# Performance work log

Hardware: AMD Instinct MI355X
Metric: run time of the kernel (lower is better)

## Reference

```python
import jax, jax.numpy as jnp
import numpy as np

B, N, C, NC = 16, 49, 512, 12  # batch, spatial tokens, channels, num AU classes
EPS = 1e-5


def bn(h, axes):
    # torch BatchNorm (training mode, gamma=1, beta=0): biased batch stats
    m = h.mean(axes, keepdims=True)
    v = h.var(axes, keepdims=True)
    return (h - m) * jax.lax.rsqrt(v + EPS)


def cross_attn(y, x, qw, qb, kw, kb, vw, vb):
    # CrossAttn: q from y, k/v from x; attention over the token (N) axis
    q = y @ qw.T + qb            # (..., N, C//2)
    k = x @ kw.T + kb
    v = x @ vw.T + vb            # (..., N, C)
    scale = (C // 2) ** -0.5
    attn = jax.nn.softmax(jnp.einsum('...ij,...kj->...ik', q, k) * scale, axis=-1)
    return attn @ v


def _gnn_block(x, edge, A, Bm, E, U, V):
    # One ME-GraphAU GCN message-passing block.
    # x: (B, NC, C) node feats; edge: (B, NC*NC, C), edge (i,j) stored at i*NC+j
    b = x.shape[0]
    Vix = x @ A.T   # gathered at end node j of each edge
    Vjx = x @ Bm.T  # gathered at start node i of each edge
    msg = (Vjx[:, :, None, :] + Vix[:, None, :, :]).reshape(b, NC * NC, C) + edge @ E.T
    edge = edge + jax.nn.relu(bn(msg, (0, 2)))              # bne: per-edge-slot stats
    e = jax.nn.sigmoid(edge).reshape(b, NC, NC, C)
    e = jax.nn.softmax(e, axis=2)                            # softmax over target j
    Ujx = x @ V.T                                            # start-node features
    agg = (e * Ujx[:, :, None, :]).sum(axis=1) / NC          # sum over source i -> node j
    xn = x @ U.T + agg
    x = jax.nn.relu(x + bn(xn, (0, 2)))                      # bnv: per-class stats
    return x, edge


def _forward(x, cls_w, cls_b, attn_qw, attn_qb, attn_kw, attn_kb, attn_vw, attn_vb,
             ep_w, ep_b, gnn_w, mlp_w1, mlp_b1, mlp_w2, mlp_b2, mlp_w3, mlp_b3,
             final_w, final_b):
    b = x.shape[0]
    # per-class LinearBlocks, batched: (B, NC, N, C)
    h = jnp.einsum('bnc,koc->bkno', x, cls_w) + cls_b[None, :, None, :]
    f_u = jax.nn.relu(bn(h, (0, 2)))           # each class has its own BN over (B, N)
    f_v = f_u.mean(-2)                          # (B, NC, C)

    # GEM edge extractor
    g = jnp.broadcast_to(x[:, None], (b, NC, N, C))
    feat = cross_attn(f_u, g, attn_qw[0], attn_qb[0], attn_kw[0], attn_kb[0], attn_vw[0], attn_vb[0])
    # feat_end[i*NC+j] = feat[i]; feat_start[i*NC+j] = feat[j]
    feat_end = jnp.broadcast_to(feat[:, :, None], (b, NC, NC, N, C)).reshape(b, NC * NC, N, C)
    feat_start = jnp.broadcast_to(feat[:, None, :], (b, NC, NC, N, C)).reshape(b, NC * NC, N, C)
    feat2 = cross_attn(feat_start, feat_end, attn_qw[1], attn_qb[1], attn_kw[1], attn_kb[1], attn_vw[1], attn_vb[1])
    edge = bn(feat2 @ ep_w.T + ep_b, (0, 2, 3))  # BatchNorm2d(NC*NC): stats over (B, N, C)
    f_e = edge.mean(-2)                           # (B, NC*NC, C)

    # two GCN message-passing blocks
    U1, V1, A1, B1, E1, U2, V2, A2, B2, E2 = gnn_w
    f_v, f_e = _gnn_block(f_v, f_e, A1, B1, E1, U1, V1)
    f_v, f_e = _gnn_block(f_v, f_e, A2, B2, E2, U2, V2)

    # vectorized pairwise class-link head (feed_type='vertex+edge'), pairs i<j in loop order
    iu, ju = np.triu_indices(NC, 1)
    edges = jnp.concatenate([f_e[:, iu * NC + ju], f_e[:, ju * NC + iu]], axis=-1)  # (B, 66, 2C)
    nodes = jnp.concatenate([f_v[:, iu], f_v[:, ju]], axis=-1)                       # (B, 66, 2C)

    def mlp(z, i):
        z = jax.nn.relu(z @ mlp_w1[i].T + mlp_b1[i])
        z = jax.nn.relu(z @ mlp_w2[i].T + mlp_b2[i])
        return z @ mlp_w3[i].T + mlp_b3[i]

    ed = mlp(edges, 0)
    nd = mlp(nodes, 1)
    return jnp.concatenate([ed, nd], axis=-1) @ final_w.T + final_b  # (B, 66, 4)


def setup_inputs() -> dict:
    key = jax.random.key(0)
    ks = jax.random.split(key, 12)

    def w(k, shape, fan_in):
        return jax.random.normal(k, shape, jnp.float32) * (2.0 / fan_in) ** 0.5

    return dict(
        x=jax.random.normal(ks[0], (B, N, C), jnp.float32),
        cls_w=w(ks[1], (NC, C, C), C),          # per-class Linear (out, in)
        cls_b=jnp.zeros((NC, C), jnp.float32),
        attn_qw=w(ks[2], (2, C // 2, C), C),    # [0]=FAM, [1]=ARM
        attn_qb=jnp.zeros((2, C // 2), jnp.float32),
        attn_kw=w(ks[3], (2, C // 2, C), C),
        attn_kb=jnp.zeros((2, C // 2), jnp.float32),
        attn_vw=w(ks[4], (2, C, C), C),
        attn_vb=jnp.zeros((2, C), jnp.float32),
        ep_w=w(ks[5], (C, C), C),               # GEM edge_proj
        ep_b=jnp.zeros((C,), jnp.float32),
        gnn_w=w(ks[6], (10, C, C), C),          # U1,V1,A1,B1,E1,U2,V2,A2,B2,E2 (no bias)
        mlp_w1=w(ks[7], (2, C, 2 * C), 2 * C),  # [0]=edge_fc_*, [1]=node_fc_*
        mlp_b1=jnp.zeros((2, C), jnp.float32),
        mlp_w2=w(ks[8], (2, C // 2, C), C),
        mlp_b2=jnp.zeros((2, C // 2), jnp.float32),
        mlp_w3=w(ks[9], (2, 4, C // 2), C // 2),
        mlp_b3=jnp.zeros((2, 4), jnp.float32),
        final_w=w(ks[10], (4, 8), 8),
        final_b=jnp.zeros((4,), jnp.float32),
    )


def reference(x, cls_w, cls_b, attn_qw, attn_qb, attn_kw, attn_kb, attn_vw, attn_vb,
              ep_w, ep_b, gnn_w, mlp_w1, mlp_b1, mlp_w2, mlp_b2, mlp_w3, mlp_b3,
              final_w, final_b):
    return _forward(x, cls_w, cls_b, attn_qw, attn_qb, attn_kw, attn_kb, attn_vw, attn_vb,
                    ep_w, ep_b, gnn_w, mlp_w1, mlp_b1, mlp_w2, mlp_b2, mlp_w3, mlp_b3,
                    final_w, final_b)
```

## Files before the change

kernel.cpp:

```cpp
#include <hip/hip_runtime.h>

#define BN_EPS 1e-5f

typedef float f32x4 __attribute__((ext_vector_type(4)));
typedef short s16x8 __attribute__((ext_vector_type(8)));

__device__ __forceinline__ short f2bf(float f) {
    unsigned u = __builtin_bit_cast(unsigned, f);
    u = (u + 0x7fffu + ((u >> 16) & 1u)) >> 16;
    return (short)u;
}

__global__ __launch_bounds__(256) void cvt_multi_kernel(
    const float* __restrict__ s0, const float* __restrict__ s1, const float* __restrict__ s2,
    const float* __restrict__ s3, const float* __restrict__ s4, const float* __restrict__ s5,
    const float* __restrict__ s6, const float* __restrict__ s7, const float* __restrict__ s8,
    short* __restrict__ d0, short* __restrict__ d1, short* __restrict__ d2,
    short* __restrict__ d3, short* __restrict__ d4, short* __restrict__ d5,
    short* __restrict__ d6, short* __restrict__ d7, short* __restrict__ d8)
{
    int idx = blockIdx.x * 256 + threadIdx.x;
    const float* src; short* dst; int local;
    if      (idx <   50176) { src = s0; dst = d0; local = idx; }
    else if (idx <  443392) { src = s1; dst = d1; local = idx -   50176; }
    else if (idx <  476160) { src = s2; dst = d2; local = idx -  443392; }
    else if (idx <  508928) { src = s3; dst = d3; local = idx -  476160; }
    else if (idx <  574464) { src = s4; dst = d4; local = idx -  508928; }
    else if (idx <  607232) { src = s5; dst = d5; local = idx -  574464; }
    else if (idx <  934912) { src = s6; dst = d6; local = idx -  607232; }
    else if (idx < 1065984) { src = s7; dst = d7; local = idx -  934912; }
    else if (idx < 1098752) { src = s8; dst = d8; local = idx - 1065984; }
    else return;
    const float4* s4p = reinterpret_cast<const float4*>(src) + (size_t)local * 2;
    float4 a = s4p[0], b = s4p[1];
    s16x8 v;
    v[0] = f2bf(a.x); v[1] = f2bf(a.y); v[2] = f2bf(a.z); v[3] = f2bf(a.w);
    v[4] = f2bf(b.x); v[5] = f2bf(b.y); v[6] = f2bf(b.z); v[7] = f2bf(b.w);
    reinterpret_cast<s16x8*>(dst)[local] = v;
}

template<int OMODE>
__global__ __launch_bounds__(256) void mfma_linear_kernel(
    const short* __restrict__ X, int Xstride,
    const short* __restrict__ W, int Wstride,
    const float* __restrict__ bias, int bstride,
    void* __restrict__ Yv, int Ystride,
    int R, int Cin, int Cout, int relu)
{
    const int mat = blockIdx.z;
    X += (size_t)mat * Xstride;
    W += (size_t)mat * Wstride;
    const float* bp = bias ? bias + mat * bstride : nullptr;
    float* Yf = (float*)Yv + (size_t)mat * Ystride;
    short* Ys = (short*)Yv + (size_t)mat * Ystride;

    const int r0 = blockIdx.y * 64;
    const int o0 = blockIdx.x * 64;

    __shared__ short As[64 * 40];
    __shared__ short Bs[64 * 40];

    const int tid = threadIdx.x;
    const int lane = tid & 63;
    const int wave = tid >> 6;
    const int wr = wave >> 1, wc = wave & 1;
    const int l15 = lane & 15;
    const int lk = lane >> 4;

    const int trow = tid >> 2;
    const int tseg = (tid & 3) * 8;

    f32x4 acc[2][2] = {};

    const int arow = r0 + trow;
    const bool aok = arow < R;
    const short* xrow = X + (size_t)arow * Cin + tseg;
    const short* wrow = W + (size_t)(o0 + trow) * Cin + tseg;

    for (int k0 = 0; k0 < Cin; k0 += 32) {
        s16x8 av = {};
        if (aok) av = *reinterpret_cast<const s16x8*>(xrow + k0);
        s16x8 bv = *reinterpret_cast<const s16x8*>(wrow + k0);
        *reinterpret_cast<s16x8*>(&As[trow * 40 + tseg]) = av;
        *reinterpret_cast<s16x8*>(&Bs[trow * 40 + tseg]) = bv;
        __syncthreads();

        s16x8 af[2], bf[2];
        #pragma unroll
        for (int mi = 0; mi < 2; mi++)
            af[mi] = *reinterpret_cast<const s16x8*>(&As[(wr * 32 + mi * 16 + l15) * 40 + lk * 8]);
        #pragma unroll
        for (int ni = 0; ni < 2; ni++)
            bf[ni] = *reinterpret_cast<const s16x8*>(&Bs[(wc * 32 + ni * 16 + l15) * 40 + lk * 8]);
        #pragma unroll
        for (int mi = 0; mi < 2; mi++)
            #pragma unroll
            for (int ni = 0; ni < 2; ni++)
                acc[mi][ni] = __builtin_amdgcn_mfma_f32_16x16x32_bf16(af[mi], bf[ni], acc[mi][ni], 0, 0, 0);
        __syncthreads();
    }

    #pragma unroll
    for (int mi = 0; mi < 2; mi++) {
        #pragma unroll
        for (int ni = 0; ni < 2; ni++) {
            int col = o0 + wc * 32 + ni * 16 + l15;
            int row0 = r0 + wr * 32 + mi * 16 + lk * 4;
            float bb = bp ? bp[col] : 0.f;
            #pragma unroll
            for (int r = 0; r < 4; r++) {
                int row = row0 + r;
                if (row < R) {
                    float v = acc[mi][ni][r] + bb;
                    if (relu) v = fmaxf(v, 0.f);
                    if (OMODE == 0) {
                        Yf[(size_t)row * Cout + col] = v;
                    } else if (OMODE == 1) {
                        Ys[(size_t)row * Cout + col] = f2bf(v);
                    } else {
                        int t = row / 49, n = row - t * 49;
                        Ys[((size_t)t * 512 + col) * 64 + n] = f2bf(v);
                    }
                }
            }
        }
    }
}

__global__ __launch_bounds__(256) void bn1_partial_kernel(
    const float* __restrict__ h, float* __restrict__ bsum, float* __restrict__ bsq)
{
    int k = blockIdx.x;
    int part = blockIdx.y;
    int tid = threadIdx.x;
    #pragma unroll
    for (int half = 0; half < 2; half++) {
        int o = tid + half * 256;
        const float* base = h + (size_t)k * 401408 + (size_t)part * 98 * 512 + o;
        float s = 0.f, sq = 0.f;
        #pragma unroll 7
        for (int bn = 0; bn < 98; bn++) {
            float v = base[bn * 512];
            s += v; sq += v * v;
        }
        atomicAdd(&bsum[k * 512 + o], s);
        atomicAdd(&bsq[k * 512 + o], sq);
    }
}

__global__ __launch_bounds__(256) void fu_fv_kernel(
    const float* __restrict__ h, const float* __restrict__ bsum,
    const float* __restrict__ bsq, short* __restrict__ fu_bf,
    float* __restrict__ f_v, short* __restrict__ fv_bf)
{
    int b = blockIdx.x;
    int k = blockIdx.y;
    int tid = threadIdx.x;
    #pragma unroll
    for (int half = 0; half < 2; half++) {
        int o = tid + half * 256;
        float mu = bsum[k * 512 + o] * (1.f / 784.f);
        float var = bsq[k * 512 + o] * (1.f / 784.f) - mu * mu;
        float rs = rsqrtf(var + BN_EPS);
        const float* base = h + (size_t)(k * 16 + b) * 49 * 512 + o;
        short* obase = fu_bf + (size_t)(k * 16 + b) * 49 * 512 + o;
        float acc = 0.f;
        #pragma unroll 7
        for (int n = 0; n < 49; n++) {
            float v = (base[n * 512] - mu) * rs;
            v = fmaxf(v, 0.f);
            obase[n * 512] = f2bf(v);
            acc += v;
        }
        float fvv = acc * (1.f / 49.f);
        f_v[(b * 12 + k) * 512 + o] = fvv;
        fv_bf[(b * 12 + k) * 512 + o] = f2bf(fvv);
    }
}

__global__ __launch_bounds__(256) void attn1_kernel(
    const float* __restrict__ q1,
    const float* __restrict__ k1,
    const float* __restrict__ v1,
    short* __restrict__ feat)
{
    int b = blockIdx.x;
    int k = blockIdx.y;
    __shared__ float ks[49 * 260];
    __shared__ float Pt[49 * 56];
    int tid = threadIdx.x;
    const float* kb = k1 + b * 49 * 256;
    for (int e = tid; e < 49 * 256; e += 256) ks[(e >> 8) * 260 + (e & 255)] = kb[e];
    __syncthreads();
    const float* qb = q1 + (k * 16 + b) * 49 * 256;
    for (int e = tid; e < 49 * 49; e += 256) {
        int qi = e / 49, kj = e - qi * 49;
        const float4* q4 = reinterpret_cast<const float4*>(qb + qi * 256);
        const float4* k4 = reinterpret_cast<const float4*>(ks + kj * 260);
        float s = 0.f;
        #pragma unroll 8
        for (int d = 0; d < 64; d++) {
            float4 a = q4[d], c = k4[d];
            s += a.x * c.x + a.y * c.y + a.z * c.z + a.w * c.w;
        }
        Pt[kj * 56 + qi] = s * 0.0625f;
    }
    __syncthreads();
    if (tid < 196) {
        int qi = tid >> 2, sub = tid & 3;
        float ev[13];
        float m = -1e30f;
        #pragma unroll 13
        for (int t = 0; t < 13; t++) {
            int j = sub + t * 4;
            ev[t] = (j < 49) ? Pt[j * 56 + qi] : -1e30f;
            m = fmaxf(m, ev[t]);
        }
        m = fmaxf(m, __shfl_xor(m, 1));
        m = fmaxf(m, __shfl_xor(m, 2));
        float s = 0.f;
        #pragma unroll 13
        for (int t = 0; t < 13; t++) { ev[t] = __expf(ev[t] - m); s += ev[t]; }
        s += __shfl_xor(s, 1);
        s += __shfl_xor(s, 2);
        float inv = 1.f / s;
        #pragma unroll 13
        for (int t = 0; t < 13; t++) {
            int j = sub + t * 4;
            if (j < 49) Pt[j * 56 + qi] = ev[t] * inv;
        }
    }
    __syncthreads();
    const float* vb = v1 + b * 49 * 512;
    short* fb = feat + (size_t)(k * 16 + b) * 49 * 512;
    for (int qc = 0; qc < 49; qc += 8) {
        int nq = 49 - qc; if (nq > 8) nq = 8;
        float a0[8] = {}, a1[8] = {};
        for (int kj = 0; kj < 49; kj++) {
            float v0 = vb[kj * 512 + tid];
            float v1v = vb[kj * 512 + 256 + tid];
            const float4* pr = reinterpret_cast<const float4*>(&Pt[kj * 56 + qc]);
            float4 p0 = pr[0], p1 = pr[1];
            a0[0] += p0.x * v0; a1[0] += p0.x * v1v;
            a0[1] += p0.y * v0; a1[1] += p0.y * v1v;
            a0[2] += p0.z * v0; a1[2] += p0.z * v1v;
            a0[3] += p0.w * v0; a1[3] += p0.w * v1v;
            a0[4] += p1.x * v0; a1[4] += p1.x * v1v;
            a0[5] += p1.y * v0; a1[5] += p1.y * v1v;
            a0[6] += p1.z * v0; a1[6] += p1.z * v1v;
            a0[7] += p1.w * v0; a1[7] += p1.w * v1v;
        }
        #pragma unroll 8
        for (int u = 0; u < 8; u++) {
            if (u < nq) {
                fb[(qc + u) * 512 + tid] = f2bf(a0[u]);
                fb[(qc + u) * 512 + 256 + tid] = f2bf(a1[u]);
            }
        }
    }
}

__global__ __launch_bounds__(256) void attn2_mfma_kernel(
    const short* __restrict__ q2,
    const short* __restrict__ k2,
    const short* __restrict__ w2vT,
    const float* __restrict__ ep_b,
    float* __restrict__ fe_raw,
    float* __restrict__ stats)
{
    const int b = blockIdx.x, i = blockIdx.y;
    __shared__ short Vs[512 * 64];
    __shared__ float S[64 * 68];
    __shared__ short P[64 * 88];
    const int tid = threadIdx.x;
    const int lane = tid & 63, w = tid >> 6;
    const int l15 = lane & 15, lk = lane >> 4;

    {
        const float4* src = reinterpret_cast<const float4*>(w2vT + (size_t)((i * 16 + b) * 512) * 64);
        float4* dst = reinterpret_cast<float4*>(Vs);
        #pragma unroll
        for (int it = 0; it < 16; it++) {
            int c = tid + it * 256;
            int ch = c >> 3, c8 = c & 7;
            dst[(ch << 3) | (c8 ^ (ch & 7))] = src[c];
        }
        for (int idx = tid; idx < 64 * 88; idx += 256) P[idx] = 0;
    }
    const short* kb = k2 + (size_t)((i * 16 + b) * 49) * 256;
    __syncthreads();

    for (int j = 0; j < 12; j++) {
        const short* qb = q2 + (size_t)((j * 16 + b) * 49) * 256;
        {
            int qrow = w * 16 + l15; if (qrow > 48) qrow = 48;
            f32x4 sacc[4] = {};
            #pragma unroll
            for (int ks = 0; ks < 8; ks++) {
                s16x8 aq = *reinterpret_cast<const s16x8*>(qb + (size_t)qrow * 256 + ks * 32 + lk * 8);
                #pragma unroll
                for (int ni = 0; ni < 4; ni++) {
                    int krow = ni * 16 + l15; if (krow > 48) krow = 48;
                    s16x8 bk = *reinterpret_cast<const s16x8*>(kb + (size_t)krow * 256 + ks * 32 + lk * 8);
                    sacc[ni] = __builtin_amdgcn_mfma_f32_16x16x32_bf16(aq, bk, sacc[ni], 0, 0, 0);
                }
            }
            #pragma unroll
            for (int ni = 0; ni < 4; ni++)
                #pragma unroll
                for (int r = 0; r < 4; r++)
                    S[(w * 16 + lk * 4 + r) * 68 + ni * 16 + l15] = sacc[ni][r] * 0.0625f;
        }
        __syncthreads();

        if (tid < 196) {
            int qi = tid >> 2, sub = tid & 3;
            float ev[13];
            float m = -1e30f;
            #pragma unroll 13
            for (int t = 0; t < 13; t++) {
                int kk = sub + t * 4;
                ev[t] = (kk < 49) ? S[qi * 68 + kk] : -1e30f;
                m = fmaxf(m, ev[t]);
            }
            m = fmaxf(m, __shfl_xor(m, 1));
            m = fmaxf(m, __shfl_xor(m, 2));
            float s = 0.f;
            #pragma unroll 13
            for (int t = 0; t < 13; t++) { ev[t] = __expf(ev[t] - m); s += ev[t]; }
            s += __shfl_xor(s, 1);
            s += __shfl_xor(s, 2);
            float inv = 1.f / s;
            #pragma unroll 13
            for (int t = 0; t < 13; t++) {
                int kk = sub + t * 4;
                if (kk < 49) P[qi * 88 + kk] = f2bf(ev[t] * inv);
            }
        }
        __syncthreads();

        const int slot = i * 12 + j;
        float tot = 0.f, csq = 0.f;
        #pragma unroll
        for (int half = 0; half < 2; half++) {
            const int cb = half * 256 + w * 64;
            f32x4 pac[4][4] = {};
            #pragma unroll
            for (int ks = 0; ks < 2; ks++) {
                s16x8 bv[4];
                #pragma unroll
                for (int ni = 0; ni < 4; ni++) {
                    int ch = cb + ni * 16 + l15;
                    int boff = ((ch * 64 + ks * 32 + lk * 8) * 2) ^ ((ch & 7) << 4);
                    bv[ni] = *reinterpret_cast<const s16x8*>(reinterpret_cast<const char*>(Vs) + boff);
                }
                #pragma unroll
                for (int mi = 0; mi < 4; mi++) {
                    s16x8 ap = *reinterpret_cast<const s16x8*>(&P[(mi * 16 + l15) * 88 + ks * 32 + lk * 8]);
                    #pragma unroll
                    for (int ni = 0; ni < 4; ni++)
                        pac[mi][ni] = __builtin_amdgcn_mfma_f32_16x16x32_bf16(ap, bv[ni], pac[mi][ni], 0, 0, 0);
                }
            }
            #pragma unroll
            for (int ni = 0; ni < 4; ni++) {
                int col = cb + ni * 16 + l15;
                float bias = ep_b[col];
                float cs = 0.f;
                #pragma unroll
                for (int mi = 0; mi < 4; mi++) {
                    #pragma unroll
                    for (int r = 0; r < 4; r++) {
                        int row = mi * 16 + lk * 4 + r;
                        if (row < 49) {
                            float sv = pac[mi][ni][r] + bias;
                            cs += sv; csq += sv * sv;
                        }
                    }
                }
                tot += cs;
                cs += __shfl_xor(cs, 16);
                cs += __shfl_xor(cs, 32);
                if (lk == 0)
                    fe_raw[((size_t)b * 144 + slot) * 512 + col] = cs * (1.f / 49.f);
            }
        }
        tot += __shfl_xor(tot, 1);  tot += __shfl_xor(tot, 2);  tot += __shfl_xor(tot, 4);
        tot += __shfl_xor(tot, 8);  tot += __shfl_xor(tot, 16); tot += __shfl_xor(tot, 32);
        csq += __shfl_xor(csq, 1);  csq += __shfl_xor(csq, 2);  csq += __shfl_xor(csq, 4);
        csq += __shfl_xor(csq, 8);  csq += __shfl_xor(csq, 16); csq += __shfl_xor(csq, 32);
        if (lane == 0) {
            atomicAdd(&stats[slot * 2], tot);
            atomicAdd(&stats[slot * 2 + 1], csq);
        }
    }
}

__global__ __launch_bounds__(256) void edge_fin_kernel(
    const float* __restrict__ stats, float* __restrict__ fe, short* __restrict__ fe_bf)
{
    int s = blockIdx.x;
    const float inv = 1.f / 401408.f;
    float mu = stats[s * 2] * inv;
    float var = stats[s * 2 + 1] * inv - mu * mu;
    float rs = rsqrtf(var + BN_EPS);
    int tid = threadIdx.x;
    for (int b = 0; b < 16; b++) {
        float* p = fe + (b * 144 + s) * 512;
        short* pb = fe_bf + (b * 144 + s) * 512;
        #pragma unroll
        for (int half = 0; half < 2; half++) {
            int c = tid + half * 256;
            float nv = (p[c] - mu) * rs;
            p[c] = nv;
            pb[c] = f2bf(nv);
        }
    }
}

__global__ __launch_bounds__(256) void gnn_edge_kernel(
    const float* __restrict__ nodeproj,
    const float* __restrict__ eE,
    float* __restrict__ fe, short* __restrict__ fe_bf)
{
    int s = blockIdx.x;
    int i = s / 12, j = s - i * 12;
    int tid = threadIdx.x;
    const float* Vix = nodeproj + 2 * 98304;
    const float* Vjx = nodeproj + 3 * 98304;
    __shared__ float red[256];
    float msg[32];
    float sum = 0.f, sq = 0.f;
    int idx = 0;
    for (int b = 0; b < 16; b++) {
        #pragma unroll
        for (int half = 0; half < 2; half++) {
            int c = tid + half * 256;
            float v = Vjx[(b * 12 + i) * 512 + c] + Vix[(b * 12 + j) * 512 + c]
                    + eE[(b * 144 + s) * 512 + c];
            msg[idx++] = v;
            sum += v; sq += v * v;
        }
    }
    red[tid] = sum; __syncthreads();
    for (int t = 128; t > 0; t >>= 1) { if (tid < t) red[tid] += red[tid + t]; __syncthreads(); }
    float tsum = red[0]; __syncthreads();
    red[tid] = sq; __syncthreads();
    for (int t = 128; t > 0; t >>= 1) { if (tid < t) red[tid] += red[tid + t]; __syncthreads(); }
    float tsq = red[0];
    float mu = tsum * (1.f / 8192.f);
    float var = tsq * (1.f / 8192.f) - mu * mu;
    float rs = rsqrtf(var + BN_EPS);
    idx = 0;
    for (int b = 0; b < 16; b++) {
        #pragma unroll
        for (int half = 0; half < 2; half++) {
            int c = tid + half * 256;
            int o = (b * 144 + s) * 512 + c;
            float v = fmaxf((msg[idx++] - mu) * rs, 0.f);
            float nv = fe[o] + v;
            fe[o] = nv;
            fe_bf[o] = f2bf(nv);
        }
    }
}

__global__ __launch_bounds__(256) void gnn_agg_kernel(
    const float* __restrict__ fe,
    const float* __restrict__ nodeproj,
    float* __restrict__ xn_agg)
{
    int b = blockIdx.x;
    int i = blockIdx.y;
    int tid = threadIdx.x;
    const float* Ujx = nodeproj + 98304;
    #pragma unroll
    for (int half = 0; half < 2; half++) {
        int c = tid + half * 256;
        float sg[12];
        float m = -1e30f;
        #pragma unroll
        for (int j = 0; j < 12; j++) {
            float e = fe[(b * 144 + i * 12 + j) * 512 + c];
            float sv = 1.f / (1.f + __expf(-e));
            sg[j] = sv;
            m = fmaxf(m, sv);
        }
        float ssum = 0.f;
        #pragma unroll
        for (int j = 0; j < 12; j++) { float evv = __expf(sg[j] - m); sg[j] = evv; ssum += evv; }
        float wgt = Ujx[(b * 12 + i) * 512 + c] / ssum;
        #pragma unroll
        for (int j = 0; j < 12; j++)
            atomicAdd(&xn_agg[(b * 12 + j) * 512 + c], sg[j] * wgt);
    }
}

__global__ __launch_bounds__(256) void gnn_node_kernel(
    const float* __restrict__ xn_agg, const float* __restrict__ nodeproj,
    float* __restrict__ fv, short* __restrict__ fv_bf)
{
    int k = blockIdx.x;
    int tid = threadIdx.x;
    const float* Ux = nodeproj;
    __shared__ float red[256];
    float vals[32];
    float sum = 0.f, sq = 0.f;
    int idx = 0;
    for (int b = 0; b < 16; b++) {
        #pragma unroll
        for (int half = 0; half < 2; half++) {
            int c = tid + half * 256;
            int o = (b * 12 + k) * 512 + c;
            float v = Ux[o] + xn_agg[o] * (1.f / 12.f);
            vals[idx++] = v;
            sum += v; sq += v * v;
        }
    }
    red[tid] = sum; __syncthreads();
    for (int t = 128; t > 0; t >>= 1) { if (tid < t) red[tid] += red[tid + t]; __syncthreads(); }
    float tsum = red[0]; __syncthreads();
    red[tid] = sq; __syncthreads();
    for (int t = 128; t > 0; t >>= 1) { if (tid < t) red[tid] += red[tid + t]; __syncthreads(); }
    float tsq = red[0];
    float mu = tsum * (1.f / 8192.f);
    float var = tsq * (1.f / 8192.f) - mu * mu;
    float rs = rsqrtf(var + BN_EPS);
    idx = 0;
    for (int b = 0; b < 16; b++) {
        #pragma unroll
        for (int half = 0; half < 2; half++) {
            int c = tid + half * 256;
            int o = (b * 12 + k) * 512 + c;
            float v = (vals[idx++] - mu) * rs;
            float nv = fmaxf(fv[o] + v, 0.f);
            fv[o] = nv;
            fv_bf[o] = f2bf(nv);
        }
    }
}

__global__ __launch_bounds__(256) void pair_gather_kernel(
    const float* __restrict__ fe, const float* __restrict__ fv, short* __restrict__ pairX)
{
    int p = blockIdx.x;
    int b = blockIdx.y;
    int tid = threadIdx.x;
    int i = 0, rem = p;
    while (rem >= 11 - i) { rem -= 11 - i; i++; }
    int j = i + 1 + rem;
    short* e_out = pairX + (size_t)(b * 66 + p) * 1024;
    short* n_out = pairX + (size_t)1056 * 1024 + (size_t)(b * 66 + p) * 1024;
    const float* fe_ij = fe + (b * 144 + i * 12 + j) * 512;
    const float* fe_ji = fe + (b * 144 + j * 12 + i) * 512;
    const float* fv_i = fv + (b * 12 + i) * 512;
    const float* fv_j = fv + (b * 12 + j) * 512;
    #pragma unroll
    for (int half = 0; half < 2; half++) {
        int c = tid + half * 256;
        e_out[c] = f2bf(fe_ij[c]);
        e_out[512 + c] = f2bf(fe_ji[c]);
        n_out[c] = f2bf(fv_i[c]);
        n_out[512 + c] = f2bf(fv_j[c]);
    }
}

__global__ __launch_bounds__(256) void mlp3_kernel(
    const float* __restrict__ X,
    const float* __restrict__ w3,
    const float* __restrict__ b3,
    float* __restrict__ Y)
{
    int idx = blockIdx.x * 256 + threadIdx.x;
    if (idx >= 8448) return;
    int o = idx & 3;
    int r = (idx >> 2) % 1056;
    int m = idx / (4 * 1056);
    const float* x = X + (m * 1056 + r) * 256;
    const float* w = w3 + (m * 4 + o) * 256;
    float s = b3[m * 4 + o];
    #pragma unroll 8
    for (int c = 0; c < 256; c++) s += x[c] * w[c];
    Y[idx] = s;
}

__global__ __launch_bounds__(256) void final_kernel(
    const float* __restrict__ mid3,
    const float* __restrict__ fw,
    const float* __restrict__ fb,
    float* __restrict__ out)
{
    int idx = blockIdx.x * 256 + threadIdx.x;
    if (idx >= 4224) return;
    int o = idx & 3;
    int r = idx >> 2;
    const float* ed = mid3 + r * 4;
    const float* nd = mid3 + 1056 * 4 + r * 4;
    float s = fb[o];
    #pragma unroll
    for (int q = 0; q < 4; q++) s += ed[q] * fw[o * 8 + q];
    #pragma unroll
    for (int q = 0; q < 4; q++) s += nd[q] * fw[o * 8 + 4 + q];
    out[idx] = s;
}

extern "C" void kernel_launch(void* const* d_in, const int* in_sizes, int n_in,
                              void* d_out, int out_size, void* d_ws, size_t ws_size,
                              hipStream_t stream)
{
    const float* x      = (const float*)d_in[0];
    const float* cls_w  = (const float*)d_in[1];
    const float* cls_b  = (const float*)d_in[2];
    const float* qw     = (const float*)d_in[3];
    const float* qb     = (const float*)d_in[4];
    const float* kw     = (const float*)d_in[5];
    const float* kb     = (const float*)d_in[6];
    const float* vw     = (const float*)d_in[7];
    const float* vb     = (const float*)d_in[8];
    const float* ep_w   = (const float*)d_in[9];
    const float* ep_b   = (const float*)d_in[10];
    const float* gnn_w  = (const float*)d_in[11];
    const float* mlp_w1 = (const float*)d_in[12];
    const float* mlp_b1 = (const float*)d_in[13];
    const float* mlp_w2 = (const float*)d_in[14];
    const float* mlp_b2 = (const float*)d_in[15];
    const float* mlp_w3 = (const float*)d_in[16];
    const float* mlp_b3 = (const float*)d_in[17];
    const float* fin_w  = (const float*)d_in[18];
    const float* fin_b  = (const float*)d_in[19];
    float* out = (float*)d_out;
    float* ws = (float*)d_ws;

    float* A      = ws;
    float* q1b    = A + 4816896;
    float* k1b    = q1b + 2408448;
    float* v1b    = k1b + 200704;
    float* Bb     = v1b + 401408;
    float* Cb     = Bb + 3145728;
    float* fv     = Cb + 2408448;
    float* fvbf_f = fv + 98304;
    float* bn1m   = fvbf_f + 49152;
    float* bn1r   = bn1m + 6144;
    float* fe     = bn1r + 6144;
    float* febf_f = fe + 1179648;
    float* stats  = febf_f + 589824;
    float* xbf_f  = stats + 288;
    float* cwbf_f = xbf_f + 200704;
    float* qwbf_f = cwbf_f + 1572864;
    float* kwbf_f = qwbf_f + 131072;
    float* vwbf_f = kwbf_f + 131072;
    float* ewbf_f = vwbf_f + 262144;
    float* gwbf_f = ewbf_f + 131072;
    float* m1bf_f = gwbf_f + 1310720;
    float* m2bf_f = m1bf_f + 524288;

    short* xbf   = (short*)xbf_f;
    short* cwbf  = (short*)cwbf_f;
    short* qwbf  = (short*)qwbf_f;
    short* kwbf  = (short*)kwbf_f;
    short* vwbf  = (short*)vwbf_f;
    short* ewbf  = (short*)ewbf_f;
    short* gwbf  = (short*)gwbf_f;
    short* m1wbf = (short*)m1bf_f;
    short* m2wbf = (short*)m2bf_f;

    short* fubf   = (short*)Cb;
    short* featbf = (short*)Bb;
    short* q2bf   = (short*)A;
    short* k2bf   = (short*)A + 2408448;
    short* v2bf   = (short*)Cb;
    short* w2vT   = (short*)Bb;
    short* fvbf   = (short*)fvbf_f;
    short* febf   = (short*)febf_f;

    float* nodeproj = Cb;
    float* eE       = Cb + 393216;
    float* xn       = Cb + 1572864;
    short* pairXbf  = (short*)Cb;
    short* mid1bf   = (short*)Cb + 2162688;
    float* mid2     = Cb + 1622016;
    float* mid3     = Cb + 2162688;

    cvt_multi_kernel<<<4293, 256, 0, stream>>>(
        x, cls_w, qw, kw, vw, ep_w, gnn_w, mlp_w1, mlp_w2,
        xbf, cwbf, qwbf, kwbf, vwbf, ewbf, gwbf, m1wbf, m2wbf);

    mfma_linear_kernel<0><<<dim3(8, 13, 12), 256, 0, stream>>>(xbf, 0, cwbf, 262144, cls_b, 512,
                                                               A, 401408, 784, 512, 512, 0);
    hipMemsetAsync(bn1m, 0, 2 * 6144 * sizeof(float), stream);
    bn1_partial_kernel<<<dim3(12, 8), 256, 0, stream>>>(A, bn1m, bn1r);
    fu_fv_kernel<<<dim3(16, 12), 256, 0, stream>>>(A, bn1m, bn1r, fubf, fv, fvbf);
    mfma_linear_kernel<0><<<dim3(4, 147, 1), 256, 0, stream>>>(fubf, 0, qwbf, 0, qb, 0,
                                                               q1b, 0, 9408, 512, 256, 0);
    mfma_linear_kernel<0><<<dim3(4, 13, 1), 256, 0, stream>>>(xbf, 0, kwbf, 0, kb, 0,
                                                              k1b, 0, 784, 512, 256, 0);
    mfma_linear_kernel<0><<<dim3(8, 13, 1), 256, 0, stream>>>(xbf, 0, vwbf, 0, vb, 0,
                                                              v1b, 0, 784, 512, 512, 0);
    attn1_kernel<<<dim3(16, 12), 256, 0, stream>>>(q1b, k1b, v1b, featbf);
    mfma_linear_kernel<1><<<dim3(4, 147, 1), 256, 0, stream>>>(featbf, 0, qwbf + 131072, 0, qb + 256, 0,
                                                               q2bf, 0, 9408, 512, 256, 0);
    mfma_linear_kernel<1><<<dim3(4, 147, 1), 256, 0, stream>>>(featbf, 0, kwbf + 131072, 0, kb + 256, 0,
                                                               k2bf, 0, 9408, 512, 256, 0);
    mfma_linear_kernel<1><<<dim3(8, 147, 1), 256, 0, stream>>>(featbf, 0, vwbf + 262144, 0, vb + 512, 0,
                                                               v2bf, 0, 9408, 512, 512, 0);
    hipMemsetAsync(w2vT, 0, (size_t)12 * 16 * 512 * 64 * sizeof(short), stream);
    mfma_linear_kernel<2><<<dim3(8, 147, 1), 256, 0, stream>>>(v2bf, 0, ewbf, 0, nullptr, 0,
                                                               w2vT, 0, 9408, 512, 512, 0);
    hipMemsetAsync(stats, 0, 288 * sizeof(float), stream);
    attn2_mfma_kernel<<<dim3(16, 12), 256, 0, stream>>>(q2bf, k2bf, w2vT, ep_b, fe, stats);
    edge_fin_kernel<<<144, 256, 0, stream>>>(stats, fe, febf);

    for (int blk = 0; blk < 2; blk++) {
        const short* gw = gwbf + blk * 5 * 262144;
        mfma_linear_kernel<0><<<dim3(8, 3, 4), 256, 0, stream>>>(fvbf, 0, gw, 262144, nullptr, 0,
                                                                 nodeproj, 98304, 192, 512, 512, 0);
        mfma_linear_kernel<0><<<dim3(8, 36, 1), 256, 0, stream>>>(febf, 0, gw + 4 * 262144, 0, nullptr, 0,
                                                                  eE, 0, 2304, 512, 512, 0);
        gnn_edge_kernel<<<144, 256, 0, stream>>>(nodeproj, eE, fe, febf);
        hipMemsetAsync(xn, 0, 98304 * sizeof(float), stream);
        gnn_agg_kernel<<<dim3(16, 12), 256, 0, stream>>>(fe, nodeproj, xn);
        gnn_node_kernel<<<12, 256, 0, stream>>>(xn, nodeproj, fv, fvbf);
    }

    pair_gather_kernel<<<dim3(66, 16), 256, 0, stream>>>(fe, fv, pairXbf);
    mfma_linear_kernel<1><<<dim3(8, 17, 2), 256, 0, stream>>>(pairXbf, 1081344, m1wbf, 524288, mlp_b1, 512,
                                                              mid1bf, 540672, 1056, 1024, 512, 1);
    mfma_linear_kernel<0><<<dim3(4, 17, 2), 256, 0, stream>>>(mid1bf, 540672, m2wbf, 131072, mlp_b2, 256,
                                                              mid2, 270336, 1056, 512, 256, 1);
    mlp3_kernel<<<33, 256, 0, stream>>>(mid2, mlp_w3, mlp_b3, mid3);
    final_kernel<<<17, 256, 0, stream>>>(mid3, fin_w, fin_b, out);
}
```

Measured before the change: 481.3 us.

## Port first cross-attention to bf16 MFMA with transposed V layout

Replaces the fp32 scalar attn1 kernel with an MFMA-based version. Q, K and V projections now emit bf16, with V written transposed and zero-padded to 64 tokens. QK^T and P·V then run as 16x16x32 bf16 MFMA tiles, and the probabilities are stored as bf16 in shared memory. This removes the scalar FMA work and halves the intermediate traffic. The cost is lower precision in the attention and an extra memset for the padded V buffer.

```diff
diff --git a/kernel.cpp b/kernel.cpp
--- a/kernel.cpp
+++ b/kernel.cpp
@@ -178,42 +178,53 @@
     }
 }
 
-__global__ __launch_bounds__(256) void attn1_kernel(
-    const float* __restrict__ q1,
-    const float* __restrict__ k1,
-    const float* __restrict__ v1,
+__global__ __launch_bounds__(256) void attn1_mfma_kernel(
+    const short* __restrict__ q1,
+    const short* __restrict__ k1,
+    const short* __restrict__ v1T,
     short* __restrict__ feat)
 {
-    int b = blockIdx.x;
-    int k = blockIdx.y;
-    __shared__ float ks[49 * 260];
-    __shared__ float Pt[49 * 56];
-    int tid = threadIdx.x;
-    const float* kb = k1 + b * 49 * 256;
-    for (int e = tid; e < 49 * 256; e += 256) ks[(e >> 8) * 260 + (e & 255)] = kb[e];
+    const int b = blockIdx.x, k = blockIdx.y;
+    __shared__ float S[64 * 68];
+    __shared__ short P[64 * 88];
+    const int tid = threadIdx.x;
+    const int lane = tid & 63, w = tid >> 6;
+    const int l15 = lane & 15, lk = lane >> 4;
+
+    for (int idx = tid; idx < 64 * 88; idx += 256) P[idx] = 0;
+    const short* qb = q1 + (size_t)((k * 16 + b) * 49) * 256;
+    const short* kb = k1 + (size_t)(b * 49) * 256;
     __syncthreads();
-    const float* qb = q1 + (k * 16 + b) * 49 * 256;
-    for (int e = tid; e < 49 * 49; e += 256) {
-        int qi = e / 49, kj = e - qi * 49;
-        const float4* q4 = reinterpret_cast<const float4*>(qb + qi * 256);
-        const float4* k4 = reinterpret_cast<const float4*>(ks + kj * 260);
-        float s = 0.f;
-        #pragma unroll 8
-        for (int d = 0; d < 64; d++) {
-            float4 a = q4[d], c = k4[d];
-            s += a.x * c.x + a.y * c.y + a.z * c.z + a.w * c.w;
-        }
-        Pt[kj * 56 + qi] = s * 0.0625f;
+
+    {
+        int qrow = w * 16 + l15; if (qrow > 48) qrow = 48;
+        f32x4 sacc[4] = {};
+        #pragma unroll
+        for (int ks = 0; ks < 8; ks++) {
+            s16x8 aq = *reinterpret_cast<const s16x8*>(qb + (size_t)qrow * 256 + ks * 32 + lk * 8);
+            #pragma unroll
+            for (int ni = 0; ni < 4; ni++) {
+                int krow = ni * 16 + l15; if (krow > 48) krow = 48;
+                s16x8 bk = *reinterpret_cast<const s16x8*>(kb + (size_t)krow * 256 + ks * 32 + lk * 8);
+                sacc[ni] = __builtin_amdgcn_mfma_f32_16x16x32_bf16(aq, bk, sacc[ni], 0, 0, 0);
+            }
+        }
+        #pragma unroll
+        for (int ni = 0; ni < 4; ni++)
+            #pragma unroll
+            for (int r = 0; r < 4; r++)
+                S[(w * 16 + lk * 4 + r) * 68 + ni * 16 + l15] = sacc[ni][r] * 0.0625f;
     }
     __syncthreads();
+
     if (tid < 196) {
         int qi = tid >> 2, sub = tid & 3;
         float ev[13];
         float m = -1e30f;
         #pragma unroll 13
         for (int t = 0; t < 13; t++) {
-            int j = sub + t * 4;
-            ev[t] = (j < 49) ? Pt[j * 56 + qi] : -1e30f;
+            int kk = sub + t * 4;
+            ev[t] = (kk < 49) ? S[qi * 68 + kk] : -1e30f;
             m = fmaxf(m, ev[t]);
         }
         m = fmaxf(m, __shfl_xor(m, 1));
@@ -226,35 +237,45 @@
         float inv = 1.f / s;
         #pragma unroll 13
         for (int t = 0; t < 13; t++) {
-            int j = sub + t * 4;
-            if (j < 49) Pt[j * 56 + qi] = ev[t] * inv;
+            int kk = sub + t * 4;
+            if (kk < 49) P[qi * 88 + kk] = f2bf(ev[t] * inv);
         }
     }
     __syncthreads();
-    const float* vb = v1 + b * 49 * 512;
-    short* fb = feat + (size_t)(k * 16 + b) * 49 * 512;
-    for (int qc = 0; qc < 49; qc += 8) {
-        int nq = 49 - qc; if (nq > 8) nq = 8;
-        float a0[8] = {}, a1[8] = {};
-        for (int kj = 0; kj < 49; kj++) {
-            float v0 = vb[kj * 512 + tid];
-            float v1v = vb[kj * 512 + 256 + tid];
-            const float4* pr = reinterpret_cast<const float4*>(&Pt[kj * 56 + qc]);
-            float4 p0 = pr[0], p1 = pr[1];
-            a0[0] += p0.x * v0; a1[0] += p0.x * v1v;
-            a0[1] += p0.y * v0; a1[1] += p0.y * v1v;
-            a0[2] += p0.z * v0; a1[2] += p0.z * v1v;
-            a0[3] += p0.w * v0; a1[3] += p0.w * v1v;
-            a0[4] += p1.x * v0; a1[4] += p1.x * v1v;
-            a0[5] += p1.y * v0; a1[5] += p1.y * v1v;
-            a0[6] += p1.z * v0; a1[6] += p1.z * v1v;
-            a0[7] += p1.w * v0; a1[7] += p1.w * v1v;
-        }
-        #pragma unroll 8
-        for (int u = 0; u < 8; u++) {
-            if (u < nq) {
-                fb[(qc + u) * 512 + tid] = f2bf(a0[u]);
-                fb[(qc + u) * 512 + 256 + tid] = f2bf(a1[u]);
+
+    const short* vt = v1T + (size_t)b * 512 * 64;
+    short* fb = feat + (size_t)((k * 16 + b) * 49) * 512;
+    #pragma unroll
+    for (int half = 0; half < 2; half++) {
+        const int cb = half * 256 + w * 64;
+        f32x4 pac[4][4] = {};
+        #pragma unroll
+        for (int ks = 0; ks < 2; ks++) {
+            s16x8 bv[4];
+            #pragma unroll
+            for (int ni = 0; ni < 4; ni++) {
+                int ch = cb + ni * 16 + l15;
+                bv[ni] = *reinterpret_cast<const s16x8*>(vt + (size_t)ch * 64 + ks * 32 + lk * 8);
+            }
+            #pragma unroll
+            for (int mi = 0; mi < 4; mi++) {
+                s16x8 ap = *reinterpret_cast<const s16x8*>(&P[(mi * 16 + l15) * 88 + ks * 32 + lk * 8]);
+                #pragma unroll
+                for (int ni = 0; ni < 4; ni++)
+                    pac[mi][ni] = __builtin_amdgcn_mfma_f32_16x16x32_bf16(ap, bv[ni], pac[mi][ni], 0, 0, 0);
+            }
+        }
+        #pragma unroll
+        for (int ni = 0; ni < 4; ni++) {
+            int col = cb + ni * 16 + l15;
+            #pragma unroll
+            for (int mi = 0; mi < 4; mi++) {
+                #pragma unroll
+                for (int r = 0; r < 4; r++) {
+                    int row = mi * 16 + lk * 4 + r;
+                    if (row < 49)
+                        fb[(size_t)row * 512 + col] = f2bf(pac[mi][ni][r]);
+                }
             }
         }
     }
@@ -672,6 +693,9 @@
     short* w2vT   = (short*)Bb;
     short* fvbf   = (short*)fvbf_f;
     short* febf   = (short*)febf_f;
+    short* q1bfb  = (short*)q1b;
+    short* k1bfb  = (short*)k1b;
+    short* v1T    = (short*)v1b;
 
     float* nodeproj = Cb;
     float* eE       = Cb + 393216;
@@ -690,13 +714,14 @@
     hipMemsetAsync(bn1m, 0, 2 * 6144 * sizeof(float), stream);
     bn1_partial_kernel<<<dim3(12, 8), 256, 0, stream>>>(A, bn1m, bn1r);
     fu_fv_kernel<<<dim3(16, 12), 256, 0, stream>>>(A, bn1m, bn1r, fubf, fv, fvbf);
-    mfma_linear_kernel<0><<<dim3(4, 147, 1), 256, 0, stream>>>(fubf, 0, qwbf, 0, qb, 0,
-                                                               q1b, 0, 9408, 512, 256, 0);
-    mfma_linear_kernel<0><<<dim3(4, 13, 1), 256, 0, stream>>>(xbf, 0, kwbf, 0, kb, 0,
-                                                              k1b, 0, 784, 512, 256, 0);
-    mfma_linear_kernel<0><<<dim3(8, 13, 1), 256, 0, stream>>>(xbf, 0, vwbf, 0, vb, 0,
-                                                              v1b, 0, 784, 512, 512, 0);
-    attn1_kernel<<<dim3(16, 12), 256, 0, stream>>>(q1b, k1b, v1b, featbf);
+    mfma_linear_kernel<1><<<dim3(4, 147, 1), 256, 0, stream>>>(fubf, 0, qwbf, 0, qb, 0,
+                                                               q1bfb, 0, 9408, 512, 256, 0);
+    mfma_linear_kernel<1><<<dim3(4, 13, 1), 256, 0, stream>>>(xbf, 0, kwbf, 0, kb, 0,
+                                                              k1bfb, 0, 784, 512, 256, 0);
+    hipMemsetAsync(v1T, 0, (size_t)16 * 512 * 64 * sizeof(short), stream);
+    mfma_linear_kernel<2><<<dim3(8, 13, 1), 256, 0, stream>>>(xbf, 0, vwbf, 0, vb, 0,
+                                                              v1T, 0, 784, 512, 512, 0);
+    attn1_mfma_kernel<<<dim3(16, 12), 256, 0, stream>>>(q1bfb, k1bfb, v1T, featbf);
     mfma_linear_kernel<1><<<dim3(4, 147, 1), 256, 0, stream>>>(featbf, 0, qwbf + 131072, 0, qb + 256, 0,
                                                                q2bf, 0, 9408, 512, 256, 0);
     mfma_linear_kernel<1><<<dim3(4, 147, 1), 256, 0, stream>>>(featbf, 0, kwbf + 131072, 0, kb + 256, 0,
```

New measurement: 432.7 us (median of 3 runs). 1.11x faster.
